# Kernel optimization log

Measured on AMD Instinct MI355X. Metric: run time of the kernel, lower is better.

Reference implementation:

```python
import jax, jax.numpy as jnp
import numpy as np
import math

B, C, L, DIM = 1024, 200, 3, 512


def _sinusoidal_pe(max_len, dim):
    position = np.arange(max_len, dtype=np.float32)[:, None]
    div_term = np.exp(np.arange(0, dim, 2, dtype=np.float32) * (-math.log(10000.0) / dim))
    pe = np.zeros((max_len, dim), dtype=np.float32)
    pe[:, 0::2] = np.sin(position * div_term)
    pe[:, 1::2] = np.cos(position * div_term)
    return jnp.asarray(pe)


def setup_inputs() -> dict:
    key = jax.random.key(0)
    k1, k2, k3 = jax.random.split(key, 3)
    x = jax.random.normal(k1, (B, C), dtype=jnp.float32)
    W = jax.random.normal(k2, (C, L, DIM), dtype=jnp.float32)
    cls_token = jax.random.normal(k3, (1, 1, DIM), dtype=jnp.float32)
    pe = _sinusoidal_pe(C + 1, DIM)
    return {"x": x, "W": W, "cls_token": cls_token, "pe": pe}


def reference(x, W, cls_token, pe):
    b, c = x.shape
    _, l, d = W.shape
    pad = (l - 1) // 2
    # replicate pad along band dim, then unfold into local windows [b, c, l]
    xp = jnp.pad(x, ((0, 0), (pad, pad)), mode='edge')
    win = jnp.stack([xp[:, i:i + c] for i in range(l)], axis=-1)  # [b, c, l]
    # per-channel contraction against W[c, l, d]  (== the batched bmm in torch)
    out = jnp.einsum('bcl,cld->bcd', win, W)  # [b, c, d]
    cls = jnp.broadcast_to(cls_token, (b, 1, d))
    seq = jnp.concatenate([cls, out], axis=1)  # [b, c+1, d]
    return seq + pe[:c + 1]
```

## Files before the change

kernel.cpp:

```cpp
#include <hip/hip_runtime.h>

#define B_   1024
#define C_   200
#define L_   3
#define DIM_ 512
#define S_   (C_ + 1)

__global__ __launch_bounds__(128) void GSE_84722524880902_kernel(
    const float* __restrict__ x,
    const float* __restrict__ W,
    const float* __restrict__ cls_tok,
    const float* __restrict__ pe,
    float* __restrict__ out)
{
    const int bs = blockIdx.x;
    const int b  = bs / S_;
    const int s  = bs - b * S_;
    const int d  = threadIdx.x << 2;

    const float4 pev = *(const float4*)(pe + s * DIM_ + d);
    float4 r;

    if (s == 0) {
        const float4 cv = *(const float4*)(cls_tok + d);
        r.x = cv.x + pev.x;
        r.y = cv.y + pev.y;
        r.z = cv.z + pev.z;
        r.w = cv.w + pev.w;
    } else {
        const int c  = s - 1;
        const int cm = (c > 0)      ? c - 1 : 0;
        const int cp = (c < C_ - 1) ? c + 1 : C_ - 1;

        const float w0 = x[b * C_ + cm];
        const float w1 = x[b * C_ + c];
        const float w2 = x[b * C_ + cp];

        const float* wrow = W + c * (L_ * DIM_) + d;
        const float4 a0 = *(const float4*)(wrow + 0 * DIM_);
        const float4 a1 = *(const float4*)(wrow + 1 * DIM_);
        const float4 a2 = *(const float4*)(wrow + 2 * DIM_);

        r.x = fmaf(w0, a0.x, fmaf(w1, a1.x, fmaf(w2, a2.x, pev.x)));
        r.y = fmaf(w0, a0.y, fmaf(w1, a1.y, fmaf(w2, a2.y, pev.y)));
        r.z = fmaf(w0, a0.z, fmaf(w1, a1.z, fmaf(w2, a2.z, pev.z)));
        r.w = fmaf(w0, a0.w, fmaf(w1, a1.w, fmaf(w2, a2.w, pev.w)));
    }

    *(float4*)(out + bs * DIM_ + d) = r;
}

extern "C" void kernel_launch(void* const* d_in, const int* in_sizes, int n_in,
                              void* d_out, int out_size, void* d_ws, size_t ws_size,
                              hipStream_t stream) {
    const float* x       = (const float*)d_in[0];
    const float* W       = (const float*)d_in[1];
    const float* cls_tok = (const float*)d_in[2];
    const float* pe      = (const float*)d_in[3];
    float* out           = (float*)d_out;

    const int grid = B_ * S_;
    GSE_84722524880902_kernel<<<grid, 128, 0, stream>>>(x, W, cls_tok, pe, out);
}
```

Baseline: 436.5 us.

## Reuse W and PE rows across 16 batches per block with nontemporal stores

Remaps the grid so each block handles one channel for a group of 16 batch rows, split across two 128-thread halves. The W and positional-encoding rows are loaded once into registers and reused across 8 batch iterations per thread. This cuts redundant global loads and the number of blocks launched. Output writes become nontemporal stores to avoid polluting cache, and the CLS rows get their own small set of blocks. The kernel is write-bandwidth bound, so the gain is mostly from lower load traffic and block overhead, at some cost in parallelism per block.

```diff
diff --git a/kernel.cpp b/kernel.cpp
--- a/kernel.cpp
+++ b/kernel.cpp
@@ -6,48 +6,76 @@
 #define DIM_ 512
 #define S_   (C_ + 1)
 
-__global__ __launch_bounds__(128) void GSE_84722524880902_kernel(
+#define NB_       16
+#define NGRP_     (B_ / NB_)
+#define NBLK_C_   (C_ * NGRP_)
+#define NBLK_CLS_ NGRP_
+
+typedef float f4 __attribute__((ext_vector_type(4)));
+
+__global__ __launch_bounds__(256) void GSE_84722524880902_kernel(
     const float* __restrict__ x,
     const float* __restrict__ W,
     const float* __restrict__ cls_tok,
     const float* __restrict__ pe,
     float* __restrict__ out)
 {
-    const int bs = blockIdx.x;
-    const int b  = bs / S_;
-    const int s  = bs - b * S_;
-    const int d  = threadIdx.x << 2;
+    const int lane = threadIdx.x & 127;
+    const int bsub = threadIdx.x >> 7;
+    const int d    = lane << 2;
+    const int blk  = blockIdx.x;
 
-    const float4 pev = *(const float4*)(pe + s * DIM_ + d);
-    float4 r;
+    if (blk < NBLK_C_) {
+        const int c  = blk % C_;
+        const int bg = blk / C_;
+        const int b0 = bg * NB_ + bsub;
+        const int s  = c + 1;
 
-    if (s == 0) {
-        const float4 cv = *(const float4*)(cls_tok + d);
+        const int cm = (c > 0)      ? c - 1 : 0;
+        const int cp = (c < C_ - 1) ? c + 1 : C_ - 1;
+
+        const f4 pev = *(const f4*)(pe + s * DIM_ + d);
+        const float* wrow = W + c * (L_ * DIM_) + d;
+        const f4 a0 = *(const f4*)(wrow + 0 * DIM_);
+        const f4 a1 = *(const f4*)(wrow + 1 * DIM_);
+        const f4 a2 = *(const f4*)(wrow + 2 * DIM_);
+
+        const float* xb = x + b0 * C_;
+        f4* op = (f4*)(out + (b0 * S_ + s) * DIM_) + lane;
+
+        #pragma unroll
+        for (int i = 0; i < NB_ / 2; ++i) {
+            const float w0 = xb[cm];
+            const float w1 = xb[c];
+            const float w2 = xb[cp];
+            f4 r;
+            r.x = fmaf(w0, a0.x, fmaf(w1, a1.x, fmaf(w2, a2.x, pev.x)));
+            r.y = fmaf(w0, a0.y, fmaf(w1, a1.y, fmaf(w2, a2.y, pev.y)));
+            r.z = fmaf(w0, a0.z, fmaf(w1, a1.z, fmaf(w2, a2.z, pev.z)));
+            r.w = fmaf(w0, a0.w, fmaf(w1, a1.w, fmaf(w2, a2.w, pev.w)));
+            __builtin_nontemporal_store(r, op);
+            xb += 2 * C_;
+            op += 2 * S_ * (DIM_ / 4);
+        }
+    } else {
+        const int bg = blk - NBLK_C_;
+        const int b0 = bg * NB_ + bsub;
+
+        const f4 pev = *(const f4*)(pe + d);
+        const f4 cv  = *(const f4*)(cls_tok + d);
+        f4 r;
         r.x = cv.x + pev.x;
         r.y = cv.y + pev.y;
         r.z = cv.z + pev.z;
         r.w = cv.w + pev.w;
-    } else {
-        const int c  = s - 1;
-        const int cm = (c > 0)      ? c - 1 : 0;
-        const int cp = (c < C_ - 1) ? c + 1 : C_ - 1;
 
-        const float w0 = x[b * C_ + cm];
-        const float w1 = x[b * C_ + c];
-        const float w2 = x[b * C_ + cp];
-
-        const float* wrow = W + c * (L_ * DIM_) + d;
-        const float4 a0 = *(const float4*)(wrow + 0 * DIM_);
-        const float4 a1 = *(const float4*)(wrow + 1 * DIM_);
-        const float4 a2 = *(const float4*)(wrow + 2 * DIM_);
-
-        r.x = fmaf(w0, a0.x, fmaf(w1, a1.x, fmaf(w2, a2.x, pev.x)));
-        r.y = fmaf(w0, a0.y, fmaf(w1, a1.y, fmaf(w2, a2.y, pev.y)));
-        r.z = fmaf(w0, a0.z, fmaf(w1, a1.z, fmaf(w2, a2.z, pev.z)));
-        r.w = fmaf(w0, a0.w, fmaf(w1, a1.w, fmaf(w2, a2.w, pev.w)));
+        f4* op = (f4*)(out + b0 * S_ * DIM_) + lane;
+        #pragma unroll
+        for (int i = 0; i < NB_ / 2; ++i) {
+            __builtin_nontemporal_store(r, op);
+            op += 2 * S_ * (DIM_ / 4);
+        }
     }
-
-    *(float4*)(out + bs * DIM_ + d) = r;
 }
 
 extern "C" void kernel_launch(void* const* d_in, const int* in_sizes, int n_in,
@@ -59,6 +87,6 @@
     const float* pe      = (const float*)d_in[3];
     float* out           = (float*)d_out;
 
-    const int grid = B_ * S_;
-    GSE_84722524880902_kernel<<<grid, 128, 0, stream>>>(x, W, cls_tok, pe, out);
+    const int grid = NBLK_C_ + NBLK_CLS_;
+    GSE_84722524880902_kernel<<<grid, 256, 0, stream>>>(x, W, cls_tok, pe, out);
 }
```

Measured after the change: 407.7 us (median of 2 runs). 1.07x faster.

## Assign one batch row per block and loop over sequence positions

Applied to the files above, without the earlier changes.

Switches from one 128-thread block per (batch, position) pair to one 256-thread block per batch row. Each half of the block walks alternating sequence positions in a loop, with the half index made wave-uniform via readfirstlane. This is meant to cut the block launch and scheduling overhead of about 206K tiny blocks and to drop the per-block integer division. In exchange the grid shrinks to 1024 blocks, which lowers the parallelism available to hide memory latency in this store-bound kernel.

```diff
diff --git a/kernel.cpp b/kernel.cpp
--- a/kernel.cpp
+++ b/kernel.cpp
@@ -6,48 +6,60 @@
 #define DIM_ 512
 #define S_   (C_ + 1)
 
-__global__ __launch_bounds__(128) void GSE_84722524880902_kernel(
+
+typedef float f4 __attribute__((ext_vector_type(4)));
+
+__global__ __launch_bounds__(256) void GSE_84722524880902_kernel(
     const float* __restrict__ x,
     const float* __restrict__ W,
     const float* __restrict__ cls_tok,
     const float* __restrict__ pe,
     float* __restrict__ out)
 {
-    const int bs = blockIdx.x;
-    const int b  = bs / S_;
-    const int s  = bs - b * S_;
-    const int d  = threadIdx.x << 2;
+    const int b    = blockIdx.x;
+    const int lane = threadIdx.x & 127;
+    const int half = __builtin_amdgcn_readfirstlane(threadIdx.x >> 7);
+    const int d    = lane << 2;
 
-    const float4 pev = *(const float4*)(pe + s * DIM_ + d);
-    float4 r;
+    f4* const outb = (f4*)(out + b * (S_ * DIM_)) + lane;
+    const float* const xb = x + b * C_;
 
-    if (s == 0) {
-        const float4 cv = *(const float4*)(cls_tok + d);
-        r.x = cv.x + pev.x;
-        r.y = cv.y + pev.y;
-        r.z = cv.z + pev.z;
-        r.w = cv.w + pev.w;
-    } else {
-        const int c  = s - 1;
+    if (half == 0) {
+        const f4 cv = *(const f4*)(cls_tok + d);
+        const f4 p0 = *(const f4*)(pe + d);
+        f4 r;
+        r.x = cv.x + p0.x;
+        r.y = cv.y + p0.y;
+        r.z = cv.z + p0.z;
+        r.w = cv.w + p0.w;
+        outb[0] = r;
+    }
+
+    #pragma unroll 2
+    for (int i = 0; i < 100; ++i) {
+        const int s = 1 + 2 * i + half;
+        const int c = s - 1;
         const int cm = (c > 0)      ? c - 1 : 0;
         const int cp = (c < C_ - 1) ? c + 1 : C_ - 1;
 
-        const float w0 = x[b * C_ + cm];
-        const float w1 = x[b * C_ + c];
-        const float w2 = x[b * C_ + cp];
+        const float w0 = xb[cm];
+        const float w1 = xb[c];
+        const float w2 = xb[cp];
 
         const float* wrow = W + c * (L_ * DIM_) + d;
-        const float4 a0 = *(const float4*)(wrow + 0 * DIM_);
-        const float4 a1 = *(const float4*)(wrow + 1 * DIM_);
-        const float4 a2 = *(const float4*)(wrow + 2 * DIM_);
+        const f4 a0  = *(const f4*)(wrow + 0 * DIM_);
+        const f4 a1  = *(const f4*)(wrow + 1 * DIM_);
+        const f4 a2  = *(const f4*)(wrow + 2 * DIM_);
+        const f4 pev = *(const f4*)(pe + s * DIM_ + d);
 
+        f4 r;
         r.x = fmaf(w0, a0.x, fmaf(w1, a1.x, fmaf(w2, a2.x, pev.x)));
         r.y = fmaf(w0, a0.y, fmaf(w1, a1.y, fmaf(w2, a2.y, pev.y)));
         r.z = fmaf(w0, a0.z, fmaf(w1, a1.z, fmaf(w2, a2.z, pev.z)));
         r.w = fmaf(w0, a0.w, fmaf(w1, a1.w, fmaf(w2, a2.w, pev.w)));
+
+        outb[s * (DIM_ / 4)] = r;
     }
-
-    *(float4*)(out + bs * DIM_ + d) = r;
 }
 
 extern "C" void kernel_launch(void* const* d_in, const int* in_sizes, int n_in,
@@ -59,6 +71,5 @@
     const float* pe      = (const float*)d_in[3];
     float* out           = (float*)d_out;
 
-    const int grid = B_ * S_;
-    GSE_84722524880902_kernel<<<grid, 128, 0, stream>>>(x, W, cls_tok, pe, out);
+    GSE_84722524880902_kernel<<<B_, 256, 0, stream>>>(x, W, cls_tok, pe, out);
 }
```

Measured after the change: 471.5 us. 8.0% more time.
